# Performance work log

Measured on AMD Instinct MI355X. Metric: run time of the kernel, lower is better.

The kernel has to match this reference:

```python
import jax, jax.numpy as jnp
import numpy as np

N = 50000          # nodes
E = 800000         # edges (before self-loops)
IN_C = 128         # input feature dim
H = 4              # attention heads
C = 32             # channels per head (hidden == out == 32)
G = 64             # graphs in the batch
NEG_SLOPE_ATT = 0.2   # PyG GATConv default negative_slope
NEG_SLOPE_ACT = 0.01  # nn.LeakyReLU default


def setup_inputs() -> dict:
    key = jax.random.key(0)
    ks = jax.random.split(key, 16)
    x = jax.random.normal(ks[0], (N, IN_C), dtype=jnp.float32)
    edge_index = jax.random.randint(ks[1], (2, E), 0, N, dtype=jnp.int64)
    batch = jnp.sort(jax.random.randint(ks[2], (N,), 0, G, dtype=jnp.int64))
    def gat_params(k, din):
        k1, k2, k3 = jax.random.split(k, 3)
        W = jax.random.normal(k1, (din, H * C), dtype=jnp.float32) * (1.0 / np.sqrt(din))
        a_src = jax.random.normal(k2, (H, C), dtype=jnp.float32) * 0.1
        a_dst = jax.random.normal(k3, (H, C), dtype=jnp.float32) * 0.1
        b = jnp.zeros((H * C,), dtype=jnp.float32)
        return W, a_src, a_dst, b
    W1, a_src1, a_dst1, b1 = gat_params(ks[3], IN_C)
    W2, a_src2, a_dst2, b2 = gat_params(ks[4], H * C)
    W3, a_src3, a_dst3, b3 = gat_params(ks[5], H * C)
    return dict(x=x, edge_index=edge_index, batch=batch,
                W1=W1, a_src1=a_src1, a_dst1=a_dst1, b1=b1,
                W2=W2, a_src2=a_src2, a_dst2=a_dst2, b2=b2,
                W3=W3, a_src3=a_src3, a_dst3=a_dst3, b3=b3)


def _gat_conv(x, src, dst, W, a_src, a_dst, b):
    """PyG GATConv (concat=True, negative_slope=0.2); self-loops already in src/dst."""
    n = x.shape[0]
    h = (x @ W).reshape(n, H, C)                      # [N,H,C]
    s = jnp.einsum('nhc,hc->nh', h, a_src)            # [N,H]
    d = jnp.einsum('nhc,hc->nh', h, a_dst)            # [N,H]
    e = jax.nn.leaky_relu(s[src] + d[dst], NEG_SLOPE_ATT)  # [E',H]
    # segment softmax over incoming edges of each destination node
    m = jax.ops.segment_max(e, dst, num_segments=n)   # [N,H]
    ex = jnp.exp(e - m[dst])
    denom = jax.ops.segment_sum(ex, dst, num_segments=n)
    alpha = ex / denom[dst]                           # [E',H]
    msg = h[src] * alpha[..., None]                   # [E',H,C]
    out = jax.ops.segment_sum(msg, dst, num_segments=n).reshape(n, H * C)
    return out + b


def reference(x, edge_index, batch,
              W1, a_src1, a_dst1, b1,
              W2, a_src2, a_dst2, b2,
              W3, a_src3, a_dst3, b3):
    n = x.shape[0]
    # add self-loops (PyG GATConv default add_self_loops=True)
    loop = jnp.arange(n, dtype=edge_index.dtype)
    src = jnp.concatenate([edge_index[0], loop])
    dst = jnp.concatenate([edge_index[1], loop])
    # dropout is identity in eval mode
    h = jax.nn.leaky_relu(_gat_conv(x, src, dst, W1, a_src1, a_dst1, b1), NEG_SLOPE_ACT)
    h = jax.nn.leaky_relu(_gat_conv(h, src, dst, W2, a_src2, a_dst2, b2), NEG_SLOPE_ACT)
    h = jax.nn.leaky_relu(_gat_conv(h, src, dst, W3, a_src3, a_dst3, b3), NEG_SLOPE_ACT)
    graph_embedding = jax.ops.segment_max(h, batch, num_segments=G)  # [G, H*C]
    return (graph_embedding, h, edge_index)
```

## Files before the change

### kernel.cpp

```cpp
#include <hip/hip_runtime.h>
#include <math.h>
#include <limits.h>

#define LRELU_ATT 0.2f
#define LRELU_ACT 0.01f
#define CAP 64
#define DPB 16
#define LCAP (DPB * CAP)
#define NBMAX 512
#define TILE 8192
#define BCAP 6528
#define WPAD 136

typedef __attribute__((ext_vector_type(8))) short bf16x8;
typedef __attribute__((ext_vector_type(4))) float f32x4;

__device__ __forceinline__ float lrelu(float x, float s) { return x > 0.f ? x : x * s; }

__device__ __forceinline__ void atomicMaxF(float* addr, float val) {
    int* ai = (int*)addr;
    int old = *(volatile int*)ai;
    while (__int_as_float(old) < val) {
        int assumed = old;
        old = atomicCAS(ai, assumed, __float_as_int(val));
        if (old == assumed) break;
    }
}

__device__ __forceinline__ unsigned short f2bf(float f) {
    union { float f; unsigned u; } v; v.f = f;
    unsigned r = v.u + 0x7FFF + ((v.u >> 16) & 1);
    return (unsigned short)(r >> 16);
}
__device__ __forceinline__ float bflo(unsigned u) {
    union { unsigned u; float f; } v; v.u = u << 16;
    return v.f;
}
__device__ __forceinline__ float bfhi(unsigned u) {
    union { unsigned u; float f; } v; v.u = u & 0xffff0000u;
    return v.f;
}

__device__ __forceinline__ int* scan_incl_512(int* a, int* b, int tid, int nthr) {
    int* in = a; int* out = b;
    for (int off = 1; off < 512; off <<= 1) {
        for (int i = tid; i < 512; i += nthr)
            out[i] = in[i] + (i >= off ? in[i - off] : 0);
        __syncthreads();
        int* t = in; in = out; out = t;
    }
    return in;
}

__global__ __launch_bounds__(256) void gemm_k(const float* __restrict__ X,
                                              const float* __restrict__ Wm,
                                              const float* __restrict__ a_src,
                                              const float* __restrict__ a_dst,
                                              unsigned short* __restrict__ Hb,
                                              float* __restrict__ S,
                                              float* __restrict__ D, int n) {
    __shared__ unsigned short sWt[128 * WPAD];
    __shared__ unsigned short sXt[64 * WPAD];
    __shared__ float sa[128], sb[128];
    int tid = threadIdx.x;
    if (tid < 128) { sa[tid] = a_src[tid]; sb[tid] = a_dst[tid]; }
    int row0 = blockIdx.x * 64;
#pragma unroll
    for (int i = 0; i < 16; i++) {
        int idx4 = tid + 256 * i;
        int k = idx4 >> 5;
        int n0 = (idx4 & 31) * 4;
        float4 wv = *(const float4*)&Wm[k * 128 + n0];
        sWt[(n0 + 0) * WPAD + k] = f2bf(wv.x);
        sWt[(n0 + 1) * WPAD + k] = f2bf(wv.y);
        sWt[(n0 + 2) * WPAD + k] = f2bf(wv.z);
        sWt[(n0 + 3) * WPAD + k] = f2bf(wv.w);
    }
#pragma unroll
    for (int i = 0; i < 8; i++) {
        int idx4 = tid + 256 * i;
        int r = idx4 >> 5;
        int koff = (idx4 & 31) * 4;
        int gr = row0 + r;
        float4 xv = make_float4(0.f, 0.f, 0.f, 0.f);
        if (gr < n) xv = *(const float4*)&X[gr * 128 + koff];
        ushort4 xb;
        xb.x = f2bf(xv.x); xb.y = f2bf(xv.y); xb.z = f2bf(xv.z); xb.w = f2bf(xv.w);
        *(ushort4*)&sXt[r * WPAD + koff] = xb;
    }
    __syncthreads();
    int w = tid >> 6, l = tid & 63;
    int lr = l & 15, lk = l >> 4;
    f32x4 acc[8];
#pragma unroll
    for (int ct = 0; ct < 8; ct++) acc[ct] = (f32x4){0.f, 0.f, 0.f, 0.f};
#pragma unroll
    for (int ks = 0; ks < 4; ks++) {
        int kbase = ks * 32 + lk * 8;
        bf16x8 afrag = *(const bf16x8*)&sXt[(w * 16 + lr) * WPAD + kbase];
#pragma unroll
        for (int ct = 0; ct < 8; ct++) {
            bf16x8 bfrag = *(const bf16x8*)&sWt[(ct * 16 + lr) * WPAD + kbase];
            acc[ct] = __builtin_amdgcn_mfma_f32_16x16x32_bf16(afrag, bfrag, acc[ct], 0, 0, 0);
        }
    }
    float sp[4][4], dp[4][4];
#pragma unroll
    for (int reg = 0; reg < 4; reg++) {
#pragma unroll
        for (int hd = 0; hd < 4; hd++) {
            int c0 = (2 * hd) * 16 + lr;
            int c1 = (2 * hd + 1) * 16 + lr;
            sp[reg][hd] = acc[2 * hd][reg] * sa[c0] + acc[2 * hd + 1][reg] * sa[c1];
            dp[reg][hd] = acc[2 * hd][reg] * sb[c0] + acc[2 * hd + 1][reg] * sb[c1];
        }
    }
#pragma unroll
    for (int o = 1; o < 16; o <<= 1) {
#pragma unroll
        for (int reg = 0; reg < 4; reg++) {
#pragma unroll
            for (int hd = 0; hd < 4; hd++) {
                sp[reg][hd] += __shfl_xor(sp[reg][hd], o, 64);
                dp[reg][hd] += __shfl_xor(dp[reg][hd], o, 64);
            }
        }
    }
#pragma unroll
    for (int reg = 0; reg < 4; reg++) {
        int gr = row0 + w * 16 + lk * 4 + reg;
        if (gr < n) {
#pragma unroll
            for (int ct = 0; ct < 8; ct++)
                Hb[gr * 128 + ct * 16 + lr] = f2bf(acc[ct][reg]);
            if (lr == 0) {
                *(float4*)&S[gr * 4] = make_float4(sp[reg][0], sp[reg][1], sp[reg][2], sp[reg][3]);
                *(float4*)&D[gr * 4] = make_float4(dp[reg][0], dp[reg][1], dp[reg][2], dp[reg][3]);
            }
        }
    }
}

__global__ void fill_f_k(float* __restrict__ p, float v, int cnt) {
    int i = blockIdx.x * blockDim.x + threadIdx.x;
    if (i < cnt) p[i] = v;
}
__global__ void fill_i_k(int* __restrict__ p, int v, int cnt) {
    int i = blockIdx.x * blockDim.x + threadIdx.x;
    if (i < cnt) p[i] = v;
}

__global__ void bhist_k(const int* __restrict__ ei, int* __restrict__ bcount, int E) {
    __shared__ int h[NBMAX];
    for (int i = threadIdx.x; i < NBMAX; i += 256) h[i] = 0;
    __syncthreads();
    for (int e = blockIdx.x * blockDim.x + threadIdx.x; e < E; e += gridDim.x * blockDim.x)
        atomicAdd(&h[ei[E + e] >> 7], 1);
    __syncthreads();
    for (int i = threadIdx.x; i < NBMAX; i += 256)
        if (h[i]) atomicAdd(&bcount[i], h[i]);
}

__global__ void bscan_k(const int* __restrict__ bcount, int* __restrict__ bbase,
                        int* __restrict__ cursor, int NB) {
    __shared__ int sa[512], sb[512];
    int tid = threadIdx.x;
    for (int i = tid; i < 512; i += 256) sa[i] = (i < NB) ? bcount[i] : 0;
    __syncthreads();
    int* inc = scan_incl_512(sa, sb, tid, 256);
    for (int i = tid; i < NB; i += 256) {
        int ex = i ? inc[i - 1] : 0;
        bbase[i] = ex;
        cursor[i] = ex;
    }
    if (tid == 0) bbase[NB] = inc[NB - 1];
}

__global__ __launch_bounds__(256) void bin_scatter_k(const int* __restrict__ ei,
                                                     int* __restrict__ cursor,
                                                     unsigned* __restrict__ binned, int E) {
    __shared__ int hist[NBMAX], excl[NBMAX], curl[NBMAX], gbase[NBMAX];
    __shared__ int sa[512], sb[512];
    __shared__ unsigned staged[TILE];
    int tid = threadIdx.x;
    int e0 = blockIdx.x * TILE;
    for (int i = tid; i < NBMAX; i += 256) hist[i] = 0;
    __syncthreads();
    unsigned keys[TILE / 256];
#pragma unroll
    for (int j = 0; j < TILE / 256; j++) {
        int e = e0 + j * 256 + tid;
        if (e < E) {
            unsigned dst = (unsigned)ei[E + e];
            unsigned src = (unsigned)ei[e];
            unsigned k = (dst << 16) | src;
            keys[j] = k;
            atomicAdd(&hist[k >> 23], 1);
        } else keys[j] = 0xFFFFFFFFu;
    }
    __syncthreads();
    for (int i = tid; i < 512; i += 256) sa[i] = hist[i];
    __syncthreads();
    int* inc = scan_incl_512(sa, sb, tid, 256);
    for (int i = tid; i < NBMAX; i += 256) {
        int ex = i ? inc[i - 1] : 0;
        excl[i] = ex;
        curl[i] = ex;
    }
    __syncthreads();
#pragma unroll
    for (int j = 0; j < TILE / 256; j++) {
        unsigned k = keys[j];
        if (k != 0xFFFFFFFFu) {
            int b = k >> 23;
            int p = atomicAdd(&curl[b], 1);
            staged[p] = k;
        }
    }
    __syncthreads();
    for (int i = tid; i < NBMAX; i += 256) {
        int cnt = hist[i];
        if (cnt) gbase[i] = atomicAdd(&cursor[i], cnt);
    }
    __syncthreads();
    int total = inc[511];
    for (int p = tid; p < total; p += 256) {
        unsigned k = staged[p];
        int b = k >> 23;
        binned[gbase[b] + (p - excl[b])] = k;
    }
}

__global__ __launch_bounds__(1024) void bucket_csr_k(const unsigned* __restrict__ binned,
                                                     const int* __restrict__ bbase,
                                                     int* __restrict__ rowptr,
                                                     int* __restrict__ csr,
                                                     int n, int NB) {
    __shared__ int outL[BCAP];
    __shared__ int sa[512], sb[512];
    __shared__ int lbase[129], cur[128];
    int b = blockIdx.x;
    int tid = threadIdx.x;
    int dst0 = b << 7;
    int ndst = min(128, n - dst0);
    int ebase = bbase[b], ecnt = bbase[b + 1] - ebase;
    for (int i = tid; i < 512; i += 1024) sa[i] = (i < ndst) ? 1 : 0;
    __syncthreads();
    for (int p = tid; p < ecnt; p += 1024) {
        int ld = (int)(binned[ebase + p] >> 16) - dst0;
        atomicAdd(&sa[ld], 1);
    }
    __syncthreads();
    int* inc = scan_incl_512(sa, sb, tid, 1024);
    for (int i = tid; i < ndst; i += 1024) {
        int ex = i ? inc[i - 1] : 0;
        lbase[i] = ex;
        cur[i] = ex;
    }
    if (tid == 0) lbase[ndst] = inc[ndst - 1];
    __syncthreads();
    int total = lbase[ndst];
    for (int i = tid; i < ndst; i += 1024) {
        int p = atomicAdd(&cur[i], 1);
        outL[p] = dst0 + i;
    }
    for (int p = tid; p < ecnt; p += 1024) {
        unsigned k = binned[ebase + p];
        int ld = (int)(k >> 16) - dst0;
        int pos = atomicAdd(&cur[ld], 1);
        outL[pos] = (int)(k & 0xFFFFu);
    }
    __syncthreads();
    int w = tid >> 6, lane = tid & 63;
    for (int d = w; d < ndst; d += 16) {
        int st = lbase[d], en = lbase[d + 1];
        int deg = en - st;
        if (deg <= 1) continue;
        if (deg <= 64) {
            int v = (lane < deg) ? outL[st + lane] : INT_MAX;
            int r = 0;
            for (int j = 0; j < deg; j++) {
                int kj = __shfl(v, j, 64);
                r += (kj < v) || (kj == v && j < lane);
            }
            if (lane < deg) outL[st + r] = v;
        } else if (deg <= 128) {
            int v0 = (lane < deg) ? outL[st + lane] : 0;
            int v1 = (64 + lane < deg) ? outL[st + 64 + lane] : 0;
            int r0 = 0, r1 = 0;
            for (int j = 0; j < deg; j++) {
                int kj = outL[st + j];
                r0 += (kj < v0) || (kj == v0 && j < lane);
                r1 += (kj < v1) || (kj == v1 && j < 64 + lane);
            }
            if (lane < deg) outL[st + r0] = v0;
            if (64 + lane < deg) outL[st + r1] = v1;
        } else if (lane == 0) {
            for (int q = st + 1; q < en; q++) {
                int key = outL[q];
                int r = q - 1;
                while (r >= st && outL[r] > key) { outL[r + 1] = outL[r]; r--; }
                outL[r + 1] = key;
            }
        }
    }
    __syncthreads();
    int gb = ebase + dst0;
    for (int p = tid; p < total; p += 1024) csr[gb + p] = outL[p];
    for (int i = tid; i < ndst; i += 1024) rowptr[dst0 + i] = gb + lbase[i];
    if (b == NB - 1 && tid == 0) rowptr[n] = gb + total;
}

__global__ __launch_bounds__(256) void attn_agg_k(const int* __restrict__ rowptr,
                                                  const int* __restrict__ csr,
                                                  const float* __restrict__ S,
                                                  const float* __restrict__ Dv,
                                                  const unsigned short* __restrict__ Hb,
                                                  const float* __restrict__ bias,
                                                  float* __restrict__ Out, int n) {
    __shared__ float al[DPB][CAP * 4];
    __shared__ int srcs[LCAP];
    __shared__ float sm[DPB][4], srd[DPB][4], sdv[DPB][4];
    __shared__ int srp[DPB + 1];
    int tid = threadIdx.x;
    int base = blockIdx.x * DPB;
    if (tid <= DPB) {
        int idx = base + tid;
        srp[tid] = rowptr[idx > n ? n : idx];
    }
    __syncthreads();
    int st0 = srp[0];
    int etot = srp[DPB] - st0;
    for (int i = tid; i < etot && i < LCAP; i += 256) srcs[i] = csr[st0 + i];
    __syncthreads();

    {
        int g = tid >> 4;
        int l = tid & 15;
        int dst = base + g;
        if (dst < n) {
            int lst = srp[g] - st0;
            int deg = srp[g + 1] - srp[g];
            float4 dv = *(const float4*)&Dv[dst * 4];
            float4 m = make_float4(-INFINITY, -INFINITY, -INFINITY, -INFINITY);
            for (int pos = l; pos < deg; pos += 16) {
                int idx = lst + pos;
                int src = (idx < LCAP) ? srcs[idx] : csr[st0 + idx];
                float4 sv = *(const float4*)&S[src * 4];
                float4 e;
                e.x = lrelu(sv.x + dv.x, LRELU_ATT);
                e.y = lrelu(sv.y + dv.y, LRELU_ATT);
                e.z = lrelu(sv.z + dv.z, LRELU_ATT);
                e.w = lrelu(sv.w + dv.w, LRELU_ATT);
                if (pos < CAP) *(float4*)&al[g][pos * 4] = e;
                m.x = fmaxf(m.x, e.x); m.y = fmaxf(m.y, e.y);
                m.z = fmaxf(m.z, e.z); m.w = fmaxf(m.w, e.w);
            }
#pragma unroll
            for (int o = 1; o < 16; o <<= 1) {
                m.x = fmaxf(m.x, __shfl_xor(m.x, o, 64));
                m.y = fmaxf(m.y, __shfl_xor(m.y, o, 64));
                m.z = fmaxf(m.z, __shfl_xor(m.z, o, 64));
                m.w = fmaxf(m.w, __shfl_xor(m.w, o, 64));
            }
            float4 den = make_float4(0.f, 0.f, 0.f, 0.f);
            for (int pos = l; pos < deg; pos += 16) {
                float4 e;
                if (pos < CAP) e = *(const float4*)&al[g][pos * 4];
                else {
                    int idx = lst + pos;
                    int src = (idx < LCAP) ? srcs[idx] : csr[st0 + idx];
                    float4 sv = *(const float4*)&S[src * 4];
                    e.x = lrelu(sv.x + dv.x, LRELU_ATT);
                    e.y = lrelu(sv.y + dv.y, LRELU_ATT);
                    e.z = lrelu(sv.z + dv.z, LRELU_ATT);
                    e.w = lrelu(sv.w + dv.w, LRELU_ATT);
                }
                float4 ex;
                ex.x = __expf(e.x - m.x); ex.y = __expf(e.y - m.y);
                ex.z = __expf(e.z - m.z); ex.w = __expf(e.w - m.w);
                den.x += ex.x; den.y += ex.y; den.z += ex.z; den.w += ex.w;
                if (pos < CAP) *(float4*)&al[g][pos * 4] = ex;
            }
#pragma unroll
            for (int o = 1; o < 16; o <<= 1) {
                den.x += __shfl_xor(den.x, o, 64);
                den.y += __shfl_xor(den.y, o, 64);
                den.z += __shfl_xor(den.z, o, 64);
                den.w += __shfl_xor(den.w, o, 64);
            }
            float4 rd;
            rd.x = 1.f / den.x; rd.y = 1.f / den.y;
            rd.z = 1.f / den.z; rd.w = 1.f / den.w;
            int lim = deg < CAP ? deg : CAP;
            for (int pos = l; pos < lim; pos += 16) {
                float4 ex = *(const float4*)&al[g][pos * 4];
                ex.x *= rd.x; ex.y *= rd.y; ex.z *= rd.z; ex.w *= rd.w;
                *(float4*)&al[g][pos * 4] = ex;
            }
            if (l == 0) {
                *(float4*)&sm[g][0] = m;
                *(float4*)&srd[g][0] = rd;
                *(float4*)&sdv[g][0] = dv;
            }
        }
    }
    __syncthreads();

    int w = tid >> 6;
    int lane = tid & 63;
    int slot = lane >> 4;
    int l16 = lane & 15;
    int ch0 = l16 * 8;
    int hd = l16 >> 2;
#pragma unroll
    for (int j = 0; j < 4; j++) {
        int g2 = w * 4 + j;
        int dst = base + g2;
        if (dst >= n) break;
        int lst = srp[g2] - st0;
        int deg = srp[g2 + 1] - srp[g2];
        float4 a0 = make_float4(0.f, 0.f, 0.f, 0.f);
        float4 a1 = make_float4(0.f, 0.f, 0.f, 0.f);
        float4 b0 = make_float4(0.f, 0.f, 0.f, 0.f);
        float4 b1 = make_float4(0.f, 0.f, 0.f, 0.f);
        int pos = slot;
        for (; pos + 4 < deg; pos += 8) {
            int iA = lst + pos, iB = iA + 4;
            int srcA = (iA < LCAP) ? srcs[iA] : csr[st0 + iA];
            int srcB = (iB < LCAP) ? srcs[iB] : csr[st0 + iB];
            float aA = (pos < CAP) ? al[g2][pos * 4 + hd]
                : __expf(lrelu(S[srcA * 4 + hd] + sdv[g2][hd], LRELU_ATT) - sm[g2][hd]) * srd[g2][hd];
            float aB = (pos + 4 < CAP) ? al[g2][(pos + 4) * 4 + hd]
                : __expf(lrelu(S[srcB * 4 + hd] + sdv[g2][hd], LRELU_ATT) - sm[g2][hd]) * srd[g2][hd];
            uint4 hvA = *(const uint4*)&Hb[srcA * 128 + ch0];
            uint4 hvB = *(const uint4*)&Hb[srcB * 128 + ch0];
            a0.x = fmaf(aA, bflo(hvA.x), a0.x);
            a0.y = fmaf(aA, bfhi(hvA.x), a0.y);
            a0.z = fmaf(aA, bflo(hvA.y), a0.z);
            a0.w = fmaf(aA, bfhi(hvA.y), a0.w);
            a1.x = fmaf(aA, bflo(hvA.z), a1.x);
            a1.y = fmaf(aA, bfhi(hvA.z), a1.y);
            a1.z = fmaf(aA, bflo(hvA.w), a1.z);
            a1.w = fmaf(aA, bfhi(hvA.w), a1.w);
            b0.x = fmaf(aB, bflo(hvB.x), b0.x);
            b0.y = fmaf(aB, bfhi(hvB.x), b0.y);
            b0.z = fmaf(aB, bflo(hvB.y), b0.z);
            b0.w = fmaf(aB, bfhi(hvB.y), b0.w);
            b1.x = fmaf(aB, bflo(hvB.z), b1.x);
            b1.y = fmaf(aB, bfhi(hvB.z), b1.y);
            b1.z = fmaf(aB, bflo(hvB.w), b1.z);
            b1.w = fmaf(aB, bfhi(hvB.w), b1.w);
        }
        if (pos < deg) {
            int iA = lst + pos;
            int srcA = (iA < LCAP) ? srcs[iA] : csr[st0 + iA];
            float aA = (pos < CAP) ? al[g2][pos * 4 + hd]
                : __expf(lrelu(S[srcA * 4 + hd] + sdv[g2][hd], LRELU_ATT) - sm[g2][hd]) * srd[g2][hd];
            uint4 hvA = *(const uint4*)&Hb[srcA * 128 + ch0];
            a0.x = fmaf(aA, bflo(hvA.x), a0.x);
            a0.y = fmaf(aA, bfhi(hvA.x), a0.y);
            a0.z = fmaf(aA, bflo(hvA.y), a0.z);
            a0.w = fmaf(aA, bfhi(hvA.y), a0.w);
            a1.x = fmaf(aA, bflo(hvA.z), a1.x);
            a1.y = fmaf(aA, bfhi(hvA.z), a1.y);
            a1.z = fmaf(aA, bflo(hvA.w), a1.z);
            a1.w = fmaf(aA, bfhi(hvA.w), a1.w);
        }
        a0.x += b0.x; a0.y += b0.y; a0.z += b0.z; a0.w += b0.w;
        a1.x += b1.x; a1.y += b1.y; a1.z += b1.z; a1.w += b1.w;
#pragma unroll
        for (int o = 16; o <= 32; o <<= 1) {
            a0.x += __shfl_xor(a0.x, o, 64);
            a0.y += __shfl_xor(a0.y, o, 64);
            a0.z += __shfl_xor(a0.z, o, 64);
            a0.w += __shfl_xor(a0.w, o, 64);
            a1.x += __shfl_xor(a1.x, o, 64);
            a1.y += __shfl_xor(a1.y, o, 64);
            a1.z += __shfl_xor(a1.z, o, 64);
            a1.w += __shfl_xor(a1.w, o, 64);
        }
        if (slot == 0) {
            float4 c0v = *(const float4*)&bias[ch0];
            float4 c1v = *(const float4*)&bias[ch0 + 4];
            float4 o0, o1;
            o0.x = lrelu(a0.x + c0v.x, LRELU_ACT);
            o0.y = lrelu(a0.y + c0v.y, LRELU_ACT);
            o0.z = lrelu(a0.z + c0v.z, LRELU_ACT);
            o0.w = lrelu(a0.w + c0v.w, LRELU_ACT);
            o1.x = lrelu(a1.x + c1v.x, LRELU_ACT);
            o1.y = lrelu(a1.y + c1v.y, LRELU_ACT);
            o1.z = lrelu(a1.z + c1v.z, LRELU_ACT);
            o1.w = lrelu(a1.w + c1v.w, LRELU_ACT);
            *(float4*)&Out[dst * 128 + ch0] = o0;
            *(float4*)&Out[dst * 128 + ch0 + 4] = o1;
        }
    }
}

__global__ void ge_max_k(const float* __restrict__ Hf, const int* __restrict__ batch,
                         float* __restrict__ ge, int n) {
    int c = threadIdx.x & 127;
    int rh = threadIdx.x >> 7;
    int node0 = blockIdx.x * 128;
    int hi = min(node0 + 128, n);
    int gid = -1;
    float mv = -INFINITY;
    for (int r = node0 + rh; r < hi; r += 2) {
        int g = batch[r];
        if (g != gid) {
            if (gid >= 0) atomicMaxF(&ge[gid * 128 + c], mv);
            gid = g;
            mv = -INFINITY;
        }
        mv = fmaxf(mv, Hf[r * 128 + c]);
    }
    if (gid >= 0) atomicMaxF(&ge[gid * 128 + c], mv);
}

__global__ void ei_copy_k(const int* __restrict__ ei, float* __restrict__ out, int m) {
    int i = (blockIdx.x * blockDim.x + threadIdx.x) * 4;
    if (i + 3 < m) {
        int4 v = *(const int4*)&ei[i];
        float4 o = make_float4((float)v.x, (float)v.y, (float)v.z, (float)v.w);
        *(float4*)&out[i] = o;
    } else {
        for (; i < m; i++) out[i] = (float)ei[i];
    }
}

extern "C" void kernel_launch(void* const* d_in, const int* in_sizes, int n_in,
                              void* d_out, int out_size, void* d_ws, size_t ws_size,
                              hipStream_t stream) {
    const float* x = (const float*)d_in[0];
    const int* ei = (const int*)d_in[1];
    const int* batch = (const int*)d_in[2];
    const float* Wm[3]   = {(const float*)d_in[3], (const float*)d_in[7],  (const float*)d_in[11]};
    const float* asrc[3] = {(const float*)d_in[4], (const float*)d_in[8],  (const float*)d_in[12]};
    const float* adst[3] = {(const float*)d_in[5], (const float*)d_in[9],  (const float*)d_in[13]};
    const float* bias[3] = {(const float*)d_in[6], (const float*)d_in[10], (const float*)d_in[14]};

    const int n = in_sizes[2];
    const int E = in_sizes[1] / 2;
    const int ne = E + n;
    const int G = (out_size - n * 128 - 2 * E) / 128;
    const int NB = (n + 127) >> 7;

    char* w = (char*)d_ws;
    float* Xact = (float*)w;          w += (size_t)n * 128 * 4;
    unsigned short* Hb = (unsigned short*)w; w += (size_t)n * 128 * 2;
    float* S    = (float*)w; w += (size_t)n * 4 * 4;
    float* D    = (float*)w; w += (size_t)n * 4 * 4;
    int* bcount = (int*)w;   w += NBMAX * 4;
    int* bbase  = (int*)w;   w += (NBMAX + 1) * 4;
    int* cursor = (int*)w;   w += NBMAX * 4;
    int* rowptr = (int*)w;   w += (size_t)(n + 1) * 4;
    unsigned* binned = (unsigned*)w; w += (size_t)E * 4;
    int* csr    = (int*)w;   w += (size_t)ne * 4;

    float* out   = (float*)d_out;
    float* ge    = out;
    float* hout  = out + (size_t)G * 128;
    float* eiout = out + (size_t)G * 128 + (size_t)n * 128;

    fill_i_k<<<(NBMAX + 255) / 256, 256, 0, stream>>>(bcount, 0, NBMAX);
    bhist_k<<<256, 256, 0, stream>>>(ei, bcount, E);
    bscan_k<<<1, 256, 0, stream>>>(bcount, bbase, cursor, NB);
    bin_scatter_k<<<(E + TILE - 1) / TILE, 256, 0, stream>>>(ei, cursor, binned, E);
    bucket_csr_k<<<NB, 1024, 0, stream>>>(binned, bbase, rowptr, csr, n, NB);

    const float* xin = x;
    for (int L = 0; L < 3; L++) {
        gemm_k<<<(n + 63) / 64, 256, 0, stream>>>(xin, Wm[L], asrc[L], adst[L], Hb, S, D, n);
        float* xnext = (L == 2) ? hout : Xact;
        attn_agg_k<<<(n + DPB - 1) / DPB, 256, 0, stream>>>(rowptr, csr, S, D, Hb, bias[L], xnext, n);
        xin = xnext;
    }

    fill_f_k<<<(G * 128 + 255) / 256, 256, 0, stream>>>(ge, -INFINITY, G * 128);
    ge_max_k<<<(n + 127) / 128, 256, 0, stream>>>(hout, batch, ge, n);
    ei_copy_k<<<(2 * E / 4 + 255) / 256, 256, 0, stream>>>(ei, eiout, 2 * E);
}
```

Before: 308.5 us.

## Restructure GAT aggregation: 128-thread blocks, bf16 attention weights, 8 lanes per node

The attention/aggregation kernel drops from 256 to 128 threads per block. Each 8-lane group now owns one destination node, and each lane accumulates 16 channels serially over all of that node's edges, replacing the previous 4-slot split with a cross-slot shuffle reduction. Attention logits and weights are stored in shared memory as bf16 with a padded row stride, and the cached capacity per node drops to 48, which cuts LDS use and should raise occupancy. The cost is lower precision in the attention weights, a longer serial edge loop per lane with less memory-level parallelism, and more recomputation of exponentials for high-degree nodes.

Result: faster. 299.1 us (-3.0%).

```diff
diff --git a/kernel.cpp b/kernel.cpp
--- a/kernel.cpp
+++ b/kernel.cpp
@@ -4,9 +4,10 @@
 
 #define LRELU_ATT 0.2f
 #define LRELU_ACT 0.01f
-#define CAP 64
+#define CAP 48
+#define ALST (CAP * 4 + 4)
 #define DPB 16
-#define LCAP (DPB * CAP)
+#define LCAP 768
 #define NBMAX 512
 #define TILE 8192
 #define BCAP 6528
@@ -31,6 +32,10 @@
     union { float f; unsigned u; } v; v.f = f;
     unsigned r = v.u + 0x7FFF + ((v.u >> 16) & 1);
     return (unsigned short)(r >> 16);
+}
+__device__ __forceinline__ float bf2f(unsigned short u) {
+    union { unsigned u; float f; } v; v.u = ((unsigned)u) << 16;
+    return v.f;
 }
 __device__ __forceinline__ float bflo(unsigned u) {
     union { unsigned u; float f; } v; v.u = u << 16;
@@ -311,14 +316,14 @@
     if (b == NB - 1 && tid == 0) rowptr[n] = gb + total;
 }
 
-__global__ __launch_bounds__(256) void attn_agg_k(const int* __restrict__ rowptr,
+__global__ __launch_bounds__(128) void attn_agg_k(const int* __restrict__ rowptr,
                                                   const int* __restrict__ csr,
                                                   const float* __restrict__ S,
                                                   const float* __restrict__ Dv,
                                                   const unsigned short* __restrict__ Hb,
                                                   const float* __restrict__ bias,
                                                   float* __restrict__ Out, int n) {
-    __shared__ float al[DPB][CAP * 4];
+    __shared__ unsigned short al16[DPB][ALST];
     __shared__ int srcs[LCAP];
     __shared__ float sm[DPB][4], srd[DPB][4], sdv[DPB][4];
     __shared__ int srp[DPB + 1];
@@ -331,19 +336,19 @@
     __syncthreads();
     int st0 = srp[0];
     int etot = srp[DPB] - st0;
-    for (int i = tid; i < etot && i < LCAP; i += 256) srcs[i] = csr[st0 + i];
+    for (int i = tid; i < etot && i < LCAP; i += 128) srcs[i] = csr[st0 + i];
     __syncthreads();
 
     {
-        int g = tid >> 4;
-        int l = tid & 15;
+        int g = tid >> 3;
+        int l = tid & 7;
         int dst = base + g;
         if (dst < n) {
             int lst = srp[g] - st0;
             int deg = srp[g + 1] - srp[g];
             float4 dv = *(const float4*)&Dv[dst * 4];
             float4 m = make_float4(-INFINITY, -INFINITY, -INFINITY, -INFINITY);
-            for (int pos = l; pos < deg; pos += 16) {
+            for (int pos = l; pos < deg; pos += 8) {
                 int idx = lst + pos;
                 int src = (idx < LCAP) ? srcs[idx] : csr[st0 + idx];
                 float4 sv = *(const float4*)&S[src * 4];
@@ -352,22 +357,28 @@
                 e.y = lrelu(sv.y + dv.y, LRELU_ATT);
                 e.z = lrelu(sv.z + dv.z, LRELU_ATT);
                 e.w = lrelu(sv.w + dv.w, LRELU_ATT);
-                if (pos < CAP) *(float4*)&al[g][pos * 4] = e;
+                if (pos < CAP) {
+                    ushort4 eb;
+                    eb.x = f2bf(e.x); eb.y = f2bf(e.y); eb.z = f2bf(e.z); eb.w = f2bf(e.w);
+                    *(ushort4*)&al16[g][pos * 4] = eb;
+                }
                 m.x = fmaxf(m.x, e.x); m.y = fmaxf(m.y, e.y);
                 m.z = fmaxf(m.z, e.z); m.w = fmaxf(m.w, e.w);
             }
 #pragma unroll
-            for (int o = 1; o < 16; o <<= 1) {
+            for (int o = 1; o < 8; o <<= 1) {
                 m.x = fmaxf(m.x, __shfl_xor(m.x, o, 64));
                 m.y = fmaxf(m.y, __shfl_xor(m.y, o, 64));
                 m.z = fmaxf(m.z, __shfl_xor(m.z, o, 64));
                 m.w = fmaxf(m.w, __shfl_xor(m.w, o, 64));
             }
             float4 den = make_float4(0.f, 0.f, 0.f, 0.f);
-            for (int pos = l; pos < deg; pos += 16) {
+            for (int pos = l; pos < deg; pos += 8) {
                 float4 e;
-                if (pos < CAP) e = *(const float4*)&al[g][pos * 4];
-                else {
+                if (pos < CAP) {
+                    ushort4 eb = *(const ushort4*)&al16[g][pos * 4];
+                    e.x = bf2f(eb.x); e.y = bf2f(eb.y); e.z = bf2f(eb.z); e.w = bf2f(eb.w);
+                } else {
                     int idx = lst + pos;
                     int src = (idx < LCAP) ? srcs[idx] : csr[st0 + idx];
                     float4 sv = *(const float4*)&S[src * 4];
@@ -380,10 +391,14 @@
                 ex.x = __expf(e.x - m.x); ex.y = __expf(e.y - m.y);
                 ex.z = __expf(e.z - m.z); ex.w = __expf(e.w - m.w);
                 den.x += ex.x; den.y += ex.y; den.z += ex.z; den.w += ex.w;
-                if (pos < CAP) *(float4*)&al[g][pos * 4] = ex;
-            }
-#pragma unroll
-            for (int o = 1; o < 16; o <<= 1) {
+                if (pos < CAP) {
+                    ushort4 xb;
+                    xb.x = f2bf(ex.x); xb.y = f2bf(ex.y); xb.z = f2bf(ex.z); xb.w = f2bf(ex.w);
+                    *(ushort4*)&al16[g][pos * 4] = xb;
+                }
+            }
+#pragma unroll
+            for (int o = 1; o < 8; o <<= 1) {
                 den.x += __shfl_xor(den.x, o, 64);
                 den.y += __shfl_xor(den.y, o, 64);
                 den.z += __shfl_xor(den.z, o, 64);
@@ -393,10 +408,13 @@
             rd.x = 1.f / den.x; rd.y = 1.f / den.y;
             rd.z = 1.f / den.z; rd.w = 1.f / den.w;
             int lim = deg < CAP ? deg : CAP;
-            for (int pos = l; pos < lim; pos += 16) {
-                float4 ex = *(const float4*)&al[g][pos * 4];
-                ex.x *= rd.x; ex.y *= rd.y; ex.z *= rd.z; ex.w *= rd.w;
-                *(float4*)&al[g][pos * 4] = ex;
+            for (int pos = l; pos < lim; pos += 8) {
+                ushort4 xb = *(const ushort4*)&al16[g][pos * 4];
+                xb.x = f2bf(bf2f(xb.x) * rd.x);
+                xb.y = f2bf(bf2f(xb.y) * rd.y);
+                xb.z = f2bf(bf2f(xb.z) * rd.z);
+                xb.w = f2bf(bf2f(xb.w) * rd.w);
+                *(ushort4*)&al16[g][pos * 4] = xb;
             }
             if (l == 0) {
                 *(float4*)&sm[g][0] = m;
@@ -409,93 +427,63 @@
 
     int w = tid >> 6;
     int lane = tid & 63;
-    int slot = lane >> 4;
-    int l16 = lane & 15;
-    int ch0 = l16 * 8;
-    int hd = l16 >> 2;
-#pragma unroll
-    for (int j = 0; j < 4; j++) {
-        int g2 = w * 4 + j;
-        int dst = base + g2;
-        if (dst >= n) break;
-        int lst = srp[g2] - st0;
-        int deg = srp[g2 + 1] - srp[g2];
-        float4 a0 = make_float4(0.f, 0.f, 0.f, 0.f);
-        float4 a1 = make_float4(0.f, 0.f, 0.f, 0.f);
-        float4 b0 = make_float4(0.f, 0.f, 0.f, 0.f);
-        float4 b1 = make_float4(0.f, 0.f, 0.f, 0.f);
-        int pos = slot;
-        for (; pos + 4 < deg; pos += 8) {
-            int iA = lst + pos, iB = iA + 4;
-            int srcA = (iA < LCAP) ? srcs[iA] : csr[st0 + iA];
-            int srcB = (iB < LCAP) ? srcs[iB] : csr[st0 + iB];
-            float aA = (pos < CAP) ? al[g2][pos * 4 + hd]
-                : __expf(lrelu(S[srcA * 4 + hd] + sdv[g2][hd], LRELU_ATT) - sm[g2][hd]) * srd[g2][hd];
-            float aB = (pos + 4 < CAP) ? al[g2][(pos + 4) * 4 + hd]
-                : __expf(lrelu(S[srcB * 4 + hd] + sdv[g2][hd], LRELU_ATT) - sm[g2][hd]) * srd[g2][hd];
-            uint4 hvA = *(const uint4*)&Hb[srcA * 128 + ch0];
-            uint4 hvB = *(const uint4*)&Hb[srcB * 128 + ch0];
-            a0.x = fmaf(aA, bflo(hvA.x), a0.x);
-            a0.y = fmaf(aA, bfhi(hvA.x), a0.y);
-            a0.z = fmaf(aA, bflo(hvA.y), a0.z);
-            a0.w = fmaf(aA, bfhi(hvA.y), a0.w);
-            a1.x = fmaf(aA, bflo(hvA.z), a1.x);
-            a1.y = fmaf(aA, bfhi(hvA.z), a1.y);
-            a1.z = fmaf(aA, bflo(hvA.w), a1.z);
-            a1.w = fmaf(aA, bfhi(hvA.w), a1.w);
-            b0.x = fmaf(aB, bflo(hvB.x), b0.x);
-            b0.y = fmaf(aB, bfhi(hvB.x), b0.y);
-            b0.z = fmaf(aB, bflo(hvB.y), b0.z);
-            b0.w = fmaf(aB, bfhi(hvB.y), b0.w);
-            b1.x = fmaf(aB, bflo(hvB.z), b1.x);
-            b1.y = fmaf(aB, bfhi(hvB.z), b1.y);
-            b1.z = fmaf(aB, bflo(hvB.w), b1.z);
-            b1.w = fmaf(aB, bfhi(hvB.w), b1.w);
-        }
-        if (pos < deg) {
-            int iA = lst + pos;
-            int srcA = (iA < LCAP) ? srcs[iA] : csr[st0 + iA];
-            float aA = (pos < CAP) ? al[g2][pos * 4 + hd]
-                : __expf(lrelu(S[srcA * 4 + hd] + sdv[g2][hd], LRELU_ATT) - sm[g2][hd]) * srd[g2][hd];
-            uint4 hvA = *(const uint4*)&Hb[srcA * 128 + ch0];
-            a0.x = fmaf(aA, bflo(hvA.x), a0.x);
-            a0.y = fmaf(aA, bfhi(hvA.x), a0.y);
-            a0.z = fmaf(aA, bflo(hvA.y), a0.z);
-            a0.w = fmaf(aA, bfhi(hvA.y), a0.w);
-            a1.x = fmaf(aA, bflo(hvA.z), a1.x);
-            a1.y = fmaf(aA, bfhi(hvA.z), a1.y);
-            a1.z = fmaf(aA, bflo(hvA.w), a1.z);
-            a1.w = fmaf(aA, bfhi(hvA.w), a1.w);
-        }
-        a0.x += b0.x; a0.y += b0.y; a0.z += b0.z; a0.w += b0.w;
-        a1.x += b1.x; a1.y += b1.y; a1.z += b1.z; a1.w += b1.w;
-#pragma unroll
-        for (int o = 16; o <= 32; o <<= 1) {
-            a0.x += __shfl_xor(a0.x, o, 64);
-            a0.y += __shfl_xor(a0.y, o, 64);
-            a0.z += __shfl_xor(a0.z, o, 64);
-            a0.w += __shfl_xor(a0.w, o, 64);
-            a1.x += __shfl_xor(a1.x, o, 64);
-            a1.y += __shfl_xor(a1.y, o, 64);
-            a1.z += __shfl_xor(a1.z, o, 64);
-            a1.w += __shfl_xor(a1.w, o, 64);
-        }
-        if (slot == 0) {
-            float4 c0v = *(const float4*)&bias[ch0];
-            float4 c1v = *(const float4*)&bias[ch0 + 4];
-            float4 o0, o1;
-            o0.x = lrelu(a0.x + c0v.x, LRELU_ACT);
-            o0.y = lrelu(a0.y + c0v.y, LRELU_ACT);
-            o0.z = lrelu(a0.z + c0v.z, LRELU_ACT);
-            o0.w = lrelu(a0.w + c0v.w, LRELU_ACT);
-            o1.x = lrelu(a1.x + c1v.x, LRELU_ACT);
-            o1.y = lrelu(a1.y + c1v.y, LRELU_ACT);
-            o1.z = lrelu(a1.z + c1v.z, LRELU_ACT);
-            o1.w = lrelu(a1.w + c1v.w, LRELU_ACT);
-            *(float4*)&Out[dst * 128 + ch0] = o0;
-            *(float4*)&Out[dst * 128 + ch0 + 4] = o1;
-        }
-    }
+    int s = lane >> 3;
+    int p = lane & 7;
+    int g2 = w * 8 + s;
+    int dst = base + g2;
+    if (dst >= n) return;
+    int lst = srp[g2] - st0;
+    int deg = srp[g2 + 1] - srp[g2];
+    int ch0 = p * 16;
+    int hd = p >> 1;
+    float smh = sm[g2][hd], srdh = srd[g2][hd], sdvh = sdv[g2][hd];
+    float4 a0 = make_float4(0.f, 0.f, 0.f, 0.f);
+    float4 a1 = make_float4(0.f, 0.f, 0.f, 0.f);
+    float4 a2 = make_float4(0.f, 0.f, 0.f, 0.f);
+    float4 a3 = make_float4(0.f, 0.f, 0.f, 0.f);
+    for (int pos = 0; pos < deg; pos++) {
+        int idx = lst + pos;
+        int src = (idx < LCAP) ? srcs[idx] : csr[st0 + idx];
+        float a;
+        if (pos < CAP) a = bf2f(al16[g2][pos * 4 + hd]);
+        else a = __expf(lrelu(S[src * 4 + hd] + sdvh, LRELU_ATT) - smh) * srdh;
+        uint4 hA = *(const uint4*)&Hb[src * 128 + ch0];
+        uint4 hB = *(const uint4*)&Hb[src * 128 + ch0 + 8];
+        a0.x = fmaf(a, bflo(hA.x), a0.x);
+        a0.y = fmaf(a, bfhi(hA.x), a0.y);
+        a0.z = fmaf(a, bflo(hA.y), a0.z);
+        a0.w = fmaf(a, bfhi(hA.y), a0.w);
+        a1.x = fmaf(a, bflo(hA.z), a1.x);
+        a1.y = fmaf(a, bfhi(hA.z), a1.y);
+        a1.z = fmaf(a, bflo(hA.w), a1.z);
+        a1.w = fmaf(a, bfhi(hA.w), a1.w);
+        a2.x = fmaf(a, bflo(hB.x), a2.x);
+        a2.y = fmaf(a, bfhi(hB.x), a2.y);
+        a2.z = fmaf(a, bflo(hB.y), a2.z);
+        a2.w = fmaf(a, bfhi(hB.y), a2.w);
+        a3.x = fmaf(a, bflo(hB.z), a3.x);
+        a3.y = fmaf(a, bfhi(hB.z), a3.y);
+        a3.z = fmaf(a, bflo(hB.w), a3.z);
+        a3.w = fmaf(a, bfhi(hB.w), a3.w);
+    }
+    float4 b0 = *(const float4*)&bias[ch0];
+    float4 b1 = *(const float4*)&bias[ch0 + 4];
+    float4 b2 = *(const float4*)&bias[ch0 + 8];
+    float4 b3 = *(const float4*)&bias[ch0 + 12];
+    float4 o0, o1, o2, o3;
+    o0.x = lrelu(a0.x + b0.x, LRELU_ACT); o0.y = lrelu(a0.y + b0.y, LRELU_ACT);
+    o0.z = lrelu(a0.z + b0.z, LRELU_ACT); o0.w = lrelu(a0.w + b0.w, LRELU_ACT);
+    o1.x = lrelu(a1.x + b1.x, LRELU_ACT); o1.y = lrelu(a1.y + b1.y, LRELU_ACT);
+    o1.z = lrelu(a1.z + b1.z, LRELU_ACT); o1.w = lrelu(a1.w + b1.w, LRELU_ACT);
+    o2.x = lrelu(a2.x + b2.x, LRELU_ACT); o2.y = lrelu(a2.y + b2.y, LRELU_ACT);
+    o2.z = lrelu(a2.z + b2.z, LRELU_ACT); o2.w = lrelu(a2.w + b2.w, LRELU_ACT);
+    o3.x = lrelu(a3.x + b3.x, LRELU_ACT); o3.y = lrelu(a3.y + b3.y, LRELU_ACT);
+    o3.z = lrelu(a3.z + b3.z, LRELU_ACT); o3.w = lrelu(a3.w + b3.w, LRELU_ACT);
+    float* op = &Out[(size_t)dst * 128 + ch0];
+    *(float4*)&op[0] = o0;
+    *(float4*)&op[4] = o1;
+    *(float4*)&op[8] = o2;
+    *(float4*)&op[12] = o3;
 }
 
 __global__ void ge_max_k(const float* __restrict__ Hf, const int* __restrict__ batch,
@@ -573,7 +561,7 @@
     for (int L = 0; L < 3; L++) {
         gemm_k<<<(n + 63) / 64, 256, 0, stream>>>(xin, Wm[L], asrc[L], adst[L], Hb, S, D, n);
         float* xnext = (L == 2) ? hout : Xact;
-        attn_agg_k<<<(n + DPB - 1) / DPB, 256, 0, stream>>>(rowptr, csr, S, D, Hb, bias[L], xnext, n);
+        attn_agg_k<<<(n + DPB - 1) / DPB, 128, 0, stream>>>(rowptr, csr, S, D, Hb, bias[L], xnext, n);
         xin = xnext;
     }
 
```
